# Optimization experiments

Measured on AMD Instinct MI355X. Metric: run time of the kernel, lower is better.

The kernel has to match this reference:

```python
import jax, jax.numpy as jnp
import numpy as np

B = 16384      # batch of samples
D = 65         # inps columns: 64 input spins + 1 output spin y
NA = 64        # auxiliary (threshold) spins
N = D + NA     # spins entering vspin expansion: 129
M = N + N * (N - 1) // 2  # degree-<=2 spin monomials: 8385
GAMMA = 1.0

# pairwise index pattern (i < j), computed once at trace time
_II, _JJ = np.triu_indices(N, k=1)


def batch_vspin(b):
    # b: [B, N] -> [B, N + N(N-1)/2]: linear terms then all pairwise products b_i*b_j (i<j)
    return jnp.concatenate([b, b[:, _II] * b[:, _JJ]], axis=-1)


def setup_inputs() -> dict:
    key = jax.random.key(0)
    k1, k2, k3, k4 = jax.random.split(key, 4)
    inps = jax.random.normal(k1, (B, D), dtype=jnp.float32)
    thresh_w = jax.random.normal(k2, (NA, D), dtype=jnp.float32) * 0.1
    thresh_b = jax.random.normal(k3, (NA,), dtype=jnp.float32) * 0.1
    main_w = jax.random.normal(k4, (1, M), dtype=jnp.float32) * 0.02
    return {"inps": inps, "thresh_w": thresh_w, "thresh_b": thresh_b, "main_w": main_w}


def reference(inps, thresh_w, thresh_b, main_w):
    inps = inps.astype(jnp.float32)
    x = inps[:, :-1]                      # [B, D-1]
    y = inps[:, -1:]                      # [B, 1]
    i_right = jnp.concatenate([x, y], axis=-1)    # [B, D]
    i_wrong = jnp.concatenate([x, -y], axis=-1)   # [B, D]

    w1 = i_right @ thresh_w.T + thresh_b          # [B, NA]
    w2 = i_wrong @ thresh_w.T + thresh_b          # [B, NA]
    t1 = jnp.tanh(GAMMA * w1)
    t2 = jnp.tanh(GAMMA * w2)

    b1 = jnp.concatenate([i_right, t1], axis=-1)  # [B, N]
    b2 = jnp.concatenate([i_wrong, t2], axis=-1)  # [B, N]
    v1 = batch_vspin(b1)                          # [B, M]
    v2 = batch_vspin(b2)                          # [B, M]

    diff = (v1 - v2) @ main_w.T + 1.0             # [B, 1]
    int_penalty = jnp.sum((GAMMA / 300.0) * ((1.0 - t1 ** 2) ** 2 + (1.0 - t2 ** 2) ** 2))
    neut_penalty = jnp.sum((t2 * w2 - t1 * w1) ** 2)
    return (diff, int_penalty, neut_penalty)
```

## Files before the change

kernel.cpp:

```cpp
#include <hip/hip_runtime.h>

#define B_SZ 16384
#define N_SP 129
#define GRID 512
#define BLOCK 256

typedef _Float16 half8 __attribute__((ext_vector_type(8)));
typedef float float4v __attribute__((ext_vector_type(4)));

#define WS_TWY  6144
#define WS_QXY  6208
#define WS_QYT  6272
#define WS_LINT 6336
#define WS_LINY 6400
#define WS_P1   6464
#define WS_P2   6976

__device__ __forceinline__ int qidx(int i, int j) {
  return N_SP + i * (2 * N_SP - i - 1) / 2 + (j - i - 1);
}

__device__ __forceinline__ float fast_tanh(float x) {
  float xc = fminf(fmaxf(x, -15.f), 15.f);
  float e = __expf(2.f * xc);
  return 1.f - 2.f / (e + 1.f);
}

__global__ void setup_kernel(const float* __restrict__ mw, const float* __restrict__ tw,
                             float* __restrict__ wsf) {
  int t = blockIdx.x * blockDim.x + threadIdx.x;
  if (t < 12288) {
    int frag = t >> 9, e = t & 511;
    int lane = e >> 3, j = e & 7;
    int tbl = frag >> 3, tg = frag & 7;
    int kt = tg >> 2, g = tg & 3;
    int k = kt * 32 + (lane >> 4) * 8 + j;
    int n = (lane & 15) + 16 * g;
    float v;
    if (tbl == 0) {
      v = tw[n * 65 + k];
    } else if (tbl == 1) {
      v = mw[qidx(n, 65 + k)];
    } else {
      v = 0.f;
      if (n != k) {
        int a = n < k ? n : k, b = n < k ? k : n;
        v = mw[qidx(65 + a, 65 + b)];
      }
    }
    ((_Float16*)wsf)[t] = (_Float16)v;
  } else if (t < 12352) {
    int u = t - 12288; wsf[WS_TWY + u] = tw[u * 65 + 64];
  } else if (t < 12416) {
    int i = t - 12352; wsf[WS_QXY + i] = mw[qidx(i, 64)];
  } else if (t < 12480) {
    int u = t - 12416; wsf[WS_QYT + u] = mw[qidx(64, 65 + u)];
  } else if (t < 12544) {
    int u = t - 12480; wsf[WS_LINT + u] = mw[65 + u];
  } else if (t == 12544) {
    wsf[WS_LINY] = mw[64];
  }
}

__global__ __launch_bounds__(BLOCK, 2) void main_kernel(
    const float* __restrict__ inps, const float* __restrict__ tb,
    float* __restrict__ wsf, float* __restrict__ out) {
  __shared__ __align__(16) _Float16 s_x[4 * 1152];
  __shared__ __align__(16) _Float16 s_dt[4 * 1152];
  __shared__ float s_red[8];

  const int tid = threadIdx.x;
  const int l = tid & 63, wib = tid >> 6;
  const int wave = (blockIdx.x << 2) + wib;
  const int b0 = wave << 3;
  const int q = l >> 4, m = l & 15;
  const bool act = (q < 2);

  _Float16* xw = s_x + wib * 1152;
  _Float16* dw = s_dt + wib * 1152;

  const half8* fragv = (const half8*)wsf;
  half8 f_tw[8], f_qxt[8], f_qtt[8];
#pragma unroll
  for (int f = 0; f < 8; f++) {
    f_tw[f]  = fragv[f * 64 + l];
    f_qxt[f] = fragv[(8 + f) * 64 + l];
    f_qtt[f] = fragv[(16 + f) * 64 + l];
  }
  float twyv[4], tbv[4], qxyv[4], qytv[4], lintv[4];
#pragma unroll
  for (int g = 0; g < 4; g++) {
    int u = m + 16 * g;
    twyv[g] = wsf[WS_TWY + u];
    qxyv[g] = wsf[WS_QXY + u];
    qytv[g] = wsf[WS_QYT + u];
    lintv[g] = wsf[WS_LINT + u];
    tbv[g] = tb[u];
  }
  const float liny = wsf[WS_LINY];

  {
    const float4* src4 = (const float4*)(inps + b0 * 65);
    float4 v0 = src4[l];
    float4 v1 = src4[64 + l];
#pragma unroll
    for (int c = 0; c < 4; c++) {
      unsigned idx = l * 4 + c;
      unsigned row = idx / 65u, col = idx - row * 65u;
      xw[row * 72 + col] = (_Float16)((const float*)&v0)[c];
    }
#pragma unroll
    for (int c = 0; c < 4; c++) {
      unsigned idx = (64 + l) * 4 + c;
      unsigned row = idx / 65u, col = idx - row * 65u;
      xw[row * 72 + col] = (_Float16)((const float*)&v1)[c];
    }
    if (l < 2) {
      float4 v2 = src4[128 + l];
#pragma unroll
      for (int c = 0; c < 4; c++) {
        unsigned idx = (128 + l) * 4 + c;
        unsigned row = idx / 65u, col = idx - row * 65u;
        xw[row * 72 + col] = (_Float16)((const float*)&v2)[c];
      }
    }
  }
  __syncthreads();

  half8 ax[2];
#pragma unroll
  for (int t = 0; t < 2; t++)
    ax[t] = *(const half8*)(xw + m * 72 + t * 32 + q * 8);

  float4v acc[4];
#pragma unroll
  for (int g = 0; g < 4; g++) { acc[g][0] = 0.f; acc[g][1] = 0.f; acc[g][2] = 0.f; acc[g][3] = 0.f; }
#pragma unroll
  for (int g = 0; g < 4; g++)
#pragma unroll
    for (int t = 0; t < 2; t++)
      acc[g] = __builtin_amdgcn_mfma_f32_16x16x32_f16(ax[t], f_tw[t * 4 + g], acc[g], 0, 0, 0);

  float yv[4];
#pragma unroll
  for (int r = 0; r < 4; r++) yv[r] = (float)xw[(q * 4 + r) * 72 + 64];
  float dtv[4][4], stv[4][4];
  float pint = 0.f, pneut = 0.f;
#pragma unroll
  for (int g = 0; g < 4; g++)
#pragma unroll
    for (int r = 0; r < 4; r++) {
      float wpre = acc[g][r] + tbv[g];
      float w1 = wpre + twyv[g] * yv[r];
      float w2 = wpre - twyv[g] * yv[r];
      float t1 = fast_tanh(w1), t2 = fast_tanh(w2);
      float dt = t1 - t2, st = t1 + t2;
      dtv[g][r] = dt; stv[g][r] = st;
      if (act) {
        float a1 = 1.f - t1 * t1, a2 = 1.f - t2 * t2;
        pint += a1 * a1 + a2 * a2;
        float nv = t2 * w2 - t1 * w1;
        pneut += nv * nv;
        dw[(q * 4 + r) * 72 + m + 16 * g] = (_Float16)dt;
      }
    }

  half8 adt[2];
#pragma unroll
  for (int t = 0; t < 2; t++)
    adt[t] = *(const half8*)(dw + m * 72 + t * 32 + q * 8);

  float4v rxt[4], rtt[4];
#pragma unroll
  for (int g = 0; g < 4; g++) {
    rxt[g][0] = 0.f; rxt[g][1] = 0.f; rxt[g][2] = 0.f; rxt[g][3] = 0.f;
    rtt[g][0] = 0.f; rtt[g][1] = 0.f; rtt[g][2] = 0.f; rtt[g][3] = 0.f;
  }
#pragma unroll
  for (int g = 0; g < 4; g++)
#pragma unroll
    for (int t = 0; t < 2; t++) {
      rxt[g] = __builtin_amdgcn_mfma_f32_16x16x32_f16(adt[t], f_qxt[t * 4 + g], rxt[g], 0, 0, 0);
      rtt[g] = __builtin_amdgcn_mfma_f32_16x16x32_f16(adt[t], f_qtt[t * 4 + g], rtt[g], 0, 0, 0);
    }

  float creg[4] = {0.f, 0.f, 0.f, 0.f};
#pragma unroll
  for (int g = 0; g < 4; g++)
#pragma unroll
    for (int r = 0; r < 4; r++) {
      float xv = (float)xw[(q * 4 + r) * 72 + m + 16 * g];
      creg[r] += xv * (2.f * yv[r] * qxyv[g] + rxt[g][r])
               + yv[r] * stv[g][r] * qytv[g]
               + 0.5f * stv[g][r] * rtt[g][r]
               + lintv[g] * dtv[g][r];
    }
#pragma unroll
  for (int r = 0; r < 4; r++) {
    float c = creg[r];
    c += __shfl_xor(c, 1); c += __shfl_xor(c, 2);
    c += __shfl_xor(c, 4); c += __shfl_xor(c, 8);
    if (act && m == 0) out[b0 + q * 4 + r] = 1.f + 2.f * yv[r] * liny + c;
  }

#pragma unroll
  for (int off = 1; off < 64; off <<= 1) {
    pint += __shfl_xor(pint, off);
    pneut += __shfl_xor(pneut, off);
  }
  if (l == 0) { s_red[wib] = pint; s_red[4 + wib] = pneut; }
  __syncthreads();
  if (tid == 0) {
    wsf[WS_P1 + blockIdx.x] = s_red[0] + s_red[1] + s_red[2] + s_red[3];
    wsf[WS_P2 + blockIdx.x] = s_red[4] + s_red[5] + s_red[6] + s_red[7];
  }
}

__global__ __launch_bounds__(512) void reduce_kernel(const float* __restrict__ wsf,
                                                     float* __restrict__ out) {
  __shared__ float s[16];
  const int tid = threadIdx.x;
  float a = wsf[WS_P1 + tid];
  float b = wsf[WS_P2 + tid];
#pragma unroll
  for (int off = 1; off < 64; off <<= 1) {
    a += __shfl_xor(a, off);
    b += __shfl_xor(b, off);
  }
  const int w = tid >> 6, l = tid & 63;
  if (l == 0) { s[w] = a; s[8 + w] = b; }
  __syncthreads();
  if (tid == 0) {
    float sa = 0.f, sb = 0.f;
#pragma unroll
    for (int i = 0; i < 8; i++) { sa += s[i]; sb += s[8 + i]; }
    out[B_SZ] = sa * (1.f / 300.f);
    out[B_SZ + 1] = sb;
  }
}

extern "C" void kernel_launch(void* const* d_in, const int* in_sizes, int n_in,
                              void* d_out, int out_size, void* d_ws, size_t ws_size,
                              hipStream_t stream) {
  const float* inps = (const float*)d_in[0];
  const float* tw   = (const float*)d_in[1];
  const float* tb   = (const float*)d_in[2];
  const float* mw   = (const float*)d_in[3];
  float* out = (float*)d_out;
  float* wsf = (float*)d_ws;
  setup_kernel<<<50, 256, 0, stream>>>(mw, tw, wsf);
  main_kernel<<<GRID, BLOCK, 0, stream>>>(inps, tb, wsf, out);
  reduce_kernel<<<1, 512, 0, stream>>>(wsf, out);
}
```

Measured before the change: 71.21 us.

## Split each 16-sample tile across four waves by output column group

Each block now handles 16 samples, and each of its four waves computes one 16-column group of the 64 auxiliary spins. Before, each wave held all fragments for 8 samples and wasted half its MFMA rows. Weight fragments are staged once per block into shared memory instead of into 24 registers per lane. Partial row sums are combined through shared memory with an extra barrier. The grid doubles and the reduce kernel widens to 1024 threads, which adds a cooperative 24KB shared-memory load per block.

```diff
diff --git a/kernel.cpp b/kernel.cpp
--- a/kernel.cpp
+++ b/kernel.cpp
@@ -2,7 +2,7 @@
 
 #define B_SZ 16384
 #define N_SP 129
-#define GRID 512
+#define GRID 1024
 #define BLOCK 256
 
 typedef _Float16 half8 __attribute__((ext_vector_type(8)));
@@ -14,7 +14,7 @@
 #define WS_LINT 6336
 #define WS_LINY 6400
 #define WS_P1   6464
-#define WS_P2   6976
+#define WS_P2   7488
 
 __device__ __forceinline__ int qidx(int i, int j) {
   return N_SP + i * (2 * N_SP - i - 1) / 2 + (j - i - 1);
@@ -62,145 +62,106 @@
   }
 }
 
-__global__ __launch_bounds__(BLOCK, 2) void main_kernel(
+__global__ __launch_bounds__(BLOCK, 4) void main_kernel(
     const float* __restrict__ inps, const float* __restrict__ tb,
     float* __restrict__ wsf, float* __restrict__ out) {
-  __shared__ __align__(16) _Float16 s_x[4 * 1152];
-  __shared__ __align__(16) _Float16 s_dt[4 * 1152];
+  __shared__ __align__(16) _Float16 s_frag[12288];
+  __shared__ __align__(16) _Float16 s_x[1152];
+  __shared__ __align__(16) _Float16 s_dt[1152];
+  __shared__ float s_part[64];
   __shared__ float s_red[8];
 
   const int tid = threadIdx.x;
   const int l = tid & 63, wib = tid >> 6;
-  const int wave = (blockIdx.x << 2) + wib;
-  const int b0 = wave << 3;
+  const int b0 = blockIdx.x << 4;
   const int q = l >> 4, m = l & 15;
-  const bool act = (q < 2);
-
-  _Float16* xw = s_x + wib * 1152;
-  _Float16* dw = s_dt + wib * 1152;
-
-  const half8* fragv = (const half8*)wsf;
-  half8 f_tw[8], f_qxt[8], f_qtt[8];
-#pragma unroll
-  for (int f = 0; f < 8; f++) {
-    f_tw[f]  = fragv[f * 64 + l];
-    f_qxt[f] = fragv[(8 + f) * 64 + l];
-    f_qtt[f] = fragv[(16 + f) * 64 + l];
-  }
-  float twyv[4], tbv[4], qxyv[4], qytv[4], lintv[4];
-#pragma unroll
-  for (int g = 0; g < 4; g++) {
-    int u = m + 16 * g;
-    twyv[g] = wsf[WS_TWY + u];
-    qxyv[g] = wsf[WS_QXY + u];
-    qytv[g] = wsf[WS_QYT + u];
-    lintv[g] = wsf[WS_LINT + u];
-    tbv[g] = tb[u];
-  }
+  const int u = (wib << 4) + m;
+
+  {
+    const float4* wsv = (const float4*)wsf;
+    float4* dst = (float4*)s_frag;
+#pragma unroll
+    for (int i = 0; i < 6; i++) dst[tid + 256 * i] = wsv[tid + 256 * i];
+  }
+  const float twyv = wsf[WS_TWY + u];
+  const float qxyv = wsf[WS_QXY + u];
+  const float qytv = wsf[WS_QYT + u];
+  const float lintv = wsf[WS_LINT + u];
   const float liny = wsf[WS_LINY];
+  const float tbv = tb[u];
 
   {
     const float4* src4 = (const float4*)(inps + b0 * 65);
-    float4 v0 = src4[l];
-    float4 v1 = src4[64 + l];
+    float4 v = src4[tid];
 #pragma unroll
     for (int c = 0; c < 4; c++) {
-      unsigned idx = l * 4 + c;
+      unsigned idx = tid * 4 + c;
       unsigned row = idx / 65u, col = idx - row * 65u;
-      xw[row * 72 + col] = (_Float16)((const float*)&v0)[c];
+      s_x[row * 72 + col] = (_Float16)((const float*)&v)[c];
     }
-#pragma unroll
-    for (int c = 0; c < 4; c++) {
-      unsigned idx = (64 + l) * 4 + c;
-      unsigned row = idx / 65u, col = idx - row * 65u;
-      xw[row * 72 + col] = (_Float16)((const float*)&v1)[c];
-    }
-    if (l < 2) {
-      float4 v2 = src4[128 + l];
+    if (tid < 4) {
+      float4 v2 = src4[256 + tid];
 #pragma unroll
       for (int c = 0; c < 4; c++) {
-        unsigned idx = (128 + l) * 4 + c;
+        unsigned idx = (256 + tid) * 4 + c;
         unsigned row = idx / 65u, col = idx - row * 65u;
-        xw[row * 72 + col] = (_Float16)((const float*)&v2)[c];
+        s_x[row * 72 + col] = (_Float16)((const float*)&v2)[c];
       }
     }
   }
   __syncthreads();
 
-  half8 ax[2];
-#pragma unroll
-  for (int t = 0; t < 2; t++)
-    ax[t] = *(const half8*)(xw + m * 72 + t * 32 + q * 8);
-
-  float4v acc[4];
-#pragma unroll
-  for (int g = 0; g < 4; g++) { acc[g][0] = 0.f; acc[g][1] = 0.f; acc[g][2] = 0.f; acc[g][3] = 0.f; }
-#pragma unroll
-  for (int g = 0; g < 4; g++)
-#pragma unroll
-    for (int t = 0; t < 2; t++)
-      acc[g] = __builtin_amdgcn_mfma_f32_16x16x32_f16(ax[t], f_tw[t * 4 + g], acc[g], 0, 0, 0);
-
-  float yv[4];
-#pragma unroll
-  for (int r = 0; r < 4; r++) yv[r] = (float)xw[(q * 4 + r) * 72 + 64];
-  float dtv[4][4], stv[4][4];
+  const half8* fragv = (const half8*)s_frag;
+
+  half8 ax0 = *(const half8*)(s_x + m * 72 + q * 8);
+  half8 ax1 = *(const half8*)(s_x + m * 72 + 32 + q * 8);
+
+  float4v acc = {0.f, 0.f, 0.f, 0.f};
+  acc = __builtin_amdgcn_mfma_f32_16x16x32_f16(ax0, fragv[(0 + wib) * 64 + l], acc, 0, 0, 0);
+  acc = __builtin_amdgcn_mfma_f32_16x16x32_f16(ax1, fragv[(4 + wib) * 64 + l], acc, 0, 0, 0);
+
+  float yv[4], dtv[4], stv[4];
   float pint = 0.f, pneut = 0.f;
 #pragma unroll
-  for (int g = 0; g < 4; g++)
-#pragma unroll
-    for (int r = 0; r < 4; r++) {
-      float wpre = acc[g][r] + tbv[g];
-      float w1 = wpre + twyv[g] * yv[r];
-      float w2 = wpre - twyv[g] * yv[r];
-      float t1 = fast_tanh(w1), t2 = fast_tanh(w2);
-      float dt = t1 - t2, st = t1 + t2;
-      dtv[g][r] = dt; stv[g][r] = st;
-      if (act) {
-        float a1 = 1.f - t1 * t1, a2 = 1.f - t2 * t2;
-        pint += a1 * a1 + a2 * a2;
-        float nv = t2 * w2 - t1 * w1;
-        pneut += nv * nv;
-        dw[(q * 4 + r) * 72 + m + 16 * g] = (_Float16)dt;
-      }
-    }
-
-  half8 adt[2];
-#pragma unroll
-  for (int t = 0; t < 2; t++)
-    adt[t] = *(const half8*)(dw + m * 72 + t * 32 + q * 8);
-
-  float4v rxt[4], rtt[4];
-#pragma unroll
-  for (int g = 0; g < 4; g++) {
-    rxt[g][0] = 0.f; rxt[g][1] = 0.f; rxt[g][2] = 0.f; rxt[g][3] = 0.f;
-    rtt[g][0] = 0.f; rtt[g][1] = 0.f; rtt[g][2] = 0.f; rtt[g][3] = 0.f;
-  }
-#pragma unroll
-  for (int g = 0; g < 4; g++)
-#pragma unroll
-    for (int t = 0; t < 2; t++) {
-      rxt[g] = __builtin_amdgcn_mfma_f32_16x16x32_f16(adt[t], f_qxt[t * 4 + g], rxt[g], 0, 0, 0);
-      rtt[g] = __builtin_amdgcn_mfma_f32_16x16x32_f16(adt[t], f_qtt[t * 4 + g], rtt[g], 0, 0, 0);
-    }
-
-  float creg[4] = {0.f, 0.f, 0.f, 0.f};
-#pragma unroll
-  for (int g = 0; g < 4; g++)
-#pragma unroll
-    for (int r = 0; r < 4; r++) {
-      float xv = (float)xw[(q * 4 + r) * 72 + m + 16 * g];
-      creg[r] += xv * (2.f * yv[r] * qxyv[g] + rxt[g][r])
-               + yv[r] * stv[g][r] * qytv[g]
-               + 0.5f * stv[g][r] * rtt[g][r]
-               + lintv[g] * dtv[g][r];
-    }
-#pragma unroll
   for (int r = 0; r < 4; r++) {
-    float c = creg[r];
+    yv[r] = (float)s_x[(q * 4 + r) * 72 + 64];
+    float wpre = acc[r] + tbv;
+    float w1 = wpre + twyv * yv[r];
+    float w2 = wpre - twyv * yv[r];
+    float t1 = fast_tanh(w1), t2 = fast_tanh(w2);
+    dtv[r] = t1 - t2; stv[r] = t1 + t2;
+    float a1 = 1.f - t1 * t1, a2 = 1.f - t2 * t2;
+    pint += a1 * a1 + a2 * a2;
+    float nv = t2 * w2 - t1 * w1;
+    pneut += nv * nv;
+    s_dt[(q * 4 + r) * 72 + u] = (_Float16)dtv[r];
+  }
+  __syncthreads();
+
+  half8 ad0 = *(const half8*)(s_dt + m * 72 + q * 8);
+  half8 ad1 = *(const half8*)(s_dt + m * 72 + 32 + q * 8);
+
+  float4v rxt = {0.f, 0.f, 0.f, 0.f}, rtt = {0.f, 0.f, 0.f, 0.f};
+  rxt = __builtin_amdgcn_mfma_f32_16x16x32_f16(ad0, fragv[(8 + wib) * 64 + l], rxt, 0, 0, 0);
+  rxt = __builtin_amdgcn_mfma_f32_16x16x32_f16(ad1, fragv[(12 + wib) * 64 + l], rxt, 0, 0, 0);
+  rtt = __builtin_amdgcn_mfma_f32_16x16x32_f16(ad0, fragv[(16 + wib) * 64 + l], rtt, 0, 0, 0);
+  rtt = __builtin_amdgcn_mfma_f32_16x16x32_f16(ad1, fragv[(20 + wib) * 64 + l], rtt, 0, 0, 0);
+
+  float creg[4];
+#pragma unroll
+  for (int r = 0; r < 4; r++) {
+    float xv = (float)s_x[(q * 4 + r) * 72 + u];
+    float c = xv * (2.f * yv[r] * qxyv + rxt[r])
+            + yv[r] * stv[r] * qytv
+            + 0.5f * stv[r] * rtt[r]
+            + lintv * dtv[r];
     c += __shfl_xor(c, 1); c += __shfl_xor(c, 2);
     c += __shfl_xor(c, 4); c += __shfl_xor(c, 8);
-    if (act && m == 0) out[b0 + q * 4 + r] = 1.f + 2.f * yv[r] * liny + c;
+    creg[r] = c;
+  }
+  if (m == 0) {
+#pragma unroll
+    for (int r = 0; r < 4; r++) s_part[wib * 16 + q * 4 + r] = creg[r];
   }
 
 #pragma unroll
@@ -210,15 +171,21 @@
   }
   if (l == 0) { s_red[wib] = pint; s_red[4 + wib] = pneut; }
   __syncthreads();
+
+  if (tid < 16) {
+    float c = s_part[tid] + s_part[16 + tid] + s_part[32 + tid] + s_part[48 + tid];
+    float y = (float)s_x[tid * 72 + 64];
+    out[b0 + tid] = 1.f + 2.f * y * liny + c;
+  }
   if (tid == 0) {
     wsf[WS_P1 + blockIdx.x] = s_red[0] + s_red[1] + s_red[2] + s_red[3];
     wsf[WS_P2 + blockIdx.x] = s_red[4] + s_red[5] + s_red[6] + s_red[7];
   }
 }
 
-__global__ __launch_bounds__(512) void reduce_kernel(const float* __restrict__ wsf,
-                                                     float* __restrict__ out) {
-  __shared__ float s[16];
+__global__ __launch_bounds__(1024) void reduce_kernel(const float* __restrict__ wsf,
+                                                      float* __restrict__ out) {
+  __shared__ float s[32];
   const int tid = threadIdx.x;
   float a = wsf[WS_P1 + tid];
   float b = wsf[WS_P2 + tid];
@@ -228,12 +195,12 @@
     b += __shfl_xor(b, off);
   }
   const int w = tid >> 6, l = tid & 63;
-  if (l == 0) { s[w] = a; s[8 + w] = b; }
+  if (l == 0) { s[w] = a; s[16 + w] = b; }
   __syncthreads();
   if (tid == 0) {
     float sa = 0.f, sb = 0.f;
 #pragma unroll
-    for (int i = 0; i < 8; i++) { sa += s[i]; sb += s[8 + i]; }
+    for (int i = 0; i < 16; i++) { sa += s[i]; sb += s[16 + i]; }
     out[B_SZ] = sa * (1.f / 300.f);
     out[B_SZ + 1] = sb;
   }
@@ -250,5 +217,5 @@
   float* wsf = (float*)d_ws;
   setup_kernel<<<50, 256, 0, stream>>>(mw, tw, wsf);
   main_kernel<<<GRID, BLOCK, 0, stream>>>(inps, tb, wsf, out);
-  reduce_kernel<<<1, 512, 0, stream>>>(wsf, out);
-}
+  reduce_kernel<<<1, 1024, 0, stream>>>(wsf, out);
+}
```

New measurement: 69.62 us (median of 2 runs). 1.02x faster.
